# Kernel tuning notes

Measured on AMD Instinct MI355X. Metric: run time of the kernel, lower is better.

The kernel has to match this reference:

```python
import jax, jax.numpy as jnp
import numpy as np
from jax import lax

EPS = 1e-4  # BatchNorm eps from the module

def maxpool2x2(x):
    # x: [N, C, H, W] -> 2x2 max pool, stride 2, no padding
    return lax.reduce_window(x, -jnp.inf, lax.max, (1, 1, 2, 2), (1, 1, 2, 2), 'VALID')

def conv_nchw(x, w):
    return lax.conv_general_dilated(x, w, window_strides=(1, 1), padding='VALID',
                                    dimension_numbers=('NCHW', 'OIHW', 'NCHW'))

def setup_inputs() -> dict:
    key = jax.random.key(0)
    ks = jax.random.split(key, 6)
    return {
        'x':       jax.random.normal(ks[0], (8192, 1, 32, 32), dtype=jnp.float32),
        'conv1_w': jax.random.normal(ks[1], (20, 1, 5, 5), dtype=jnp.float32) * 0.1,
        'conv2_w': jax.random.normal(ks[2], (50, 20, 5, 5), dtype=jnp.float32) * 0.1,
        'lin_w':   jax.random.normal(ks[3], (500, 1250), dtype=jnp.float32) * 0.05,
        'fc_w':    jax.random.normal(ks[4], (10, 500), dtype=jnp.float32) * 0.05,
        'fc_b':    jax.random.normal(ks[5], (10,), dtype=jnp.float32) * 0.05,
    }

def reference(x, conv1_w, conv2_w, lin_w, fc_w, fc_b):
    # --- features ---
    # Conv2d(1, 20, k=5, bias=False): [N,1,32,32] -> [N,20,28,28]
    h = conv_nchw(x, conv1_w)
    # BatchNorm2d(20, eps=1e-4, affine=False), training-mode batch stats (biased var)
    mean = jnp.mean(h, axis=(0, 2, 3), keepdims=True)
    var = jnp.var(h, axis=(0, 2, 3), keepdims=True)
    h = (h - mean) * lax.rsqrt(var + EPS)
    # ReLU + MaxPool 2x2: -> [N,20,14,14]
    h = maxpool2x2(jnp.maximum(h, 0.0))
    # Binarize(): sign of activations
    h = jnp.sign(h)
    # Conv2dBinary(20, 50, k=5): XNOR-style conv = conv with sign(W), scaled by
    # per-output-channel alpha = mean(|W|). -> [N,50,10,10]
    alpha2 = jnp.mean(jnp.abs(conv2_w), axis=(1, 2, 3)).reshape(1, -1, 1, 1)
    h = conv_nchw(h, jnp.sign(conv2_w)) * alpha2
    # Hardtanh + MaxPool 2x2: -> [N,50,5,5]
    h = maxpool2x2(jnp.clip(h, -1.0, 1.0))
    # --- dense ---
    h = h.reshape(h.shape[0], -1)  # [N, 1250], channel-major like torch.flatten
    h = jnp.sign(h)
    # LinearBinary(1250, 500): y = x @ sign(W)^T * alpha, alpha = mean(|W|, dim=1)
    alpha_l = jnp.mean(jnp.abs(lin_w), axis=1)  # [500]
    h = (h @ jnp.sign(lin_w).T) * alpha_l
    h = jnp.clip(h, -1.0, 1.0)
    # fc: Linear(500, num_classes)
    return h @ fc_w.T + fc_b
```

## Files before the change

kernel.cpp:

```cpp
#include <hip/hip_runtime.h>
#include <stdint.h>


#define NIMG 8192

typedef __attribute__((ext_vector_type(8))) _Float16 f16x8;
typedef __attribute__((ext_vector_type(16))) float f32x16;
typedef __attribute__((ext_vector_type(4))) int i32x4;
typedef __attribute__((ext_vector_type(16))) int i32x16;


__global__ __launch_bounds__(256) void prepsum_k(const float* __restrict__ lw,
                                                 const float* __restrict__ w2,
                                                 const float* __restrict__ x,
                                                 unsigned long long* __restrict__ lwp,
                                                 float* __restrict__ alpha,
                                                 i32x4* __restrict__ bg,
                                                 float* __restrict__ partial) {
  int b = blockIdx.x, tid = threadIdx.x;
  if (b < 125) {
    int wave = tid >> 6, lane = tid & 63;
    int j = b * 4 + wave;
    float pa = 0.f;
    for (int k = lane; k < 1250; k += 64) pa += fabsf(lw[j * 1250 + k]);
    for (int o = 32; o > 0; o >>= 1) pa += __shfl_down(pa, o, 64);
    if (lane == 0) alpha[j] = pa / 1250.0f;
    if (lane < 20) {
      unsigned long long m = 0;
      int base = j * 1250 + lane * 64;
      int lim = 1250 - lane * 64; if (lim > 64) lim = 64;
      for (int bb = 0; bb < lim; ++bb)
        if (lw[base + bb] > 0.f) m |= (1ull << bb);
      lwp[j * 20 + lane] = m;
    }
  } else if (b < 138) {
    int idx = (b - 125) * 256 + tid;
    if (idx < 3200) {
      int t = idx >> 7;
      int rem = idx & 127;
      int l = rem & 63;
      int nt = rem >> 6;
      int oc = nt * 32 + (l & 31);
      int hi = l >> 5;
      i32x4 o4;
#pragma unroll
      for (int wi = 0; wi < 4; ++wi) {
        int word = 0;
#pragma unroll
        for (int bb = 0; bb < 4; ++bb) {
          int k = hi * 16 + wi * 4 + bb;
          int v = 0;
          if (k < 20 && oc < 50)
            v = (w2[(oc * 20 + k) * 25 + t] > 0.f) ? 1 : -1;
          word |= (v & 0xff) << (8 * bb);
        }
        o4[wi] = word;
      }
      bg[idx] = o4;
    }
  } else {
    int sb = b - 138;
    const float4* xv = (const float4*)x + (size_t)sb * 16 * 256;
    float ax = 0.f, ay = 0.f, az = 0.f, aw = 0.f;
    for (int nn = 0; nn < 16; ++nn) {
      float4 v = xv[nn * 256 + tid];
      ax += v.x; ay += v.y; az += v.z; aw += v.w;
    }
    float4 r; r.x = ax; r.y = ay; r.z = az; r.w = aw;
    ((float4*)(partial + (size_t)sb * 1024))[tid] = r;
  }
}

__global__ __launch_bounds__(256) void reduce_k(const float* __restrict__ partial,
                                                float* __restrict__ partial2) {
  int b = blockIdx.x, tid = threadIdx.x;
  int e = (b & 3) * 256 + tid;
  int p0 = (b >> 2) * 32;
  float s = 0.f;
#pragma unroll
  for (int p = 0; p < 32; ++p) s += partial[(size_t)(p0 + p) * 1024 + e];
  partial2[(size_t)(b >> 2) * 1024 + e] = s;
}

__global__ __launch_bounds__(256) void mean_k(const float* __restrict__ partial2,
                                              const float* __restrict__ w1,
                                              float* __restrict__ mean) {
  __shared__ float Tsh[1024];
  __shared__ double U8[25][8];
  __shared__ double U[25];
  int t = threadIdx.x;
  for (int e = t; e < 1024; e += 256) {
    double s = 0.0;
#pragma unroll
    for (int b = 0; b < 16; ++b) s += (double)partial2[b * 1024 + e];
    Tsh[e] = (float)s;
  }
  __syncthreads();
  if (t < 200) {
    int tap = t >> 3, part = t & 7;
    int ky = tap / 5, kx = tap % 5;
    double s = 0.0;
    for (int p = part * 98; p < part * 98 + 98; ++p) {
      int py = p / 28, px = p % 28;
      s += (double)Tsh[(py + ky) * 32 + px + kx];
    }
    U8[tap][part] = s;
  }
  __syncthreads();
  if (t < 25) {
    double s = 0.0;
    for (int i = 0; i < 8; ++i) s += U8[t][i];
    U[t] = s;
  }
  __syncthreads();
  if (t < 20) {
    double s = 0.0;
    for (int q = 0; q < 25; ++q) s += (double)w1[t * 25 + q] * U[q];
    mean[t] = (float)(s / (8192.0 * 784.0));
  }
}

__device__ inline uint32_t pack_f16_pair(float fv) {
  _Float16 h = (_Float16)fv;
  float rem = fv - (float)h;
  _Float16 l = (_Float16)(rem * 4096.0f);
  uint32_t hb = (uint32_t)__builtin_bit_cast(unsigned short, h);
  uint32_t lb = (uint32_t)__builtin_bit_cast(unsigned short, l);
  return (hb << 16) | lb;
}

__global__ __launch_bounds__(512, 4) void conv12_k(const float* __restrict__ x,
                                                   const float* __restrict__ w1,
                                                   const float* __restrict__ mean,
                                                   const i32x4* __restrict__ bg,
                                                   const unsigned long long* __restrict__ lwp,
                                                   const float* __restrict__ alpha,
                                                   const float* __restrict__ fcw,
                                                   const float* __restrict__ fcb,
                                                   float* __restrict__ out) {
  __shared__ uint32_t xs8[8][1032];
  __shared__ uint32_t b1sh[1568];
  __shared__ __attribute__((aligned(16))) char uni[8][2048];
  int tid = threadIdx.x;
  int wave = tid >> 6, lane = tid & 63;
  int n0 = blockIdx.x * 8;
  int n = n0 + wave;

  uint32_t* xs = xs8[wave];
  {
    const float4* xin = (const float4*)(x + (size_t)n * 1024);
#pragma unroll
    for (int i = 0; i < 4; ++i) {
      int idx = i * 64 + lane;
      float4 v = xin[idx];
      float fv[4] = {v.x, v.y, v.z, v.w};
#pragma unroll
      for (int e = 0; e < 4; ++e)
        xs[4 * idx + e] = pack_f16_pair(fv[e]);
    }
    if (lane < 8) xs[1024 + lane] = 0;
  }

  int bc = lane & 31;
  int khsel = lane >> 5;
  {
    f16x8 Bh[2], Bhs[2], Bl[2];
    const int t1tab[8] = {8, 9, 18, 19, 20, 21, 22, 23};
    const _Float16 SC = (_Float16)4096.0f;
#pragma unroll
    for (int j = 0; j < 8; ++j) {
      int t0 = j + khsel * 10;
      float wv0 = (bc < 20) ? w1[bc * 25 + t0] : 0.f;
      uint32_t p0 = pack_f16_pair(wv0);
      _Float16 h0 = __builtin_bit_cast(_Float16, (unsigned short)(p0 >> 16));
      Bh[0][j] = h0;
      Bhs[0][j] = h0 * SC;
      Bl[0][j] = __builtin_bit_cast(_Float16, (unsigned short)(p0 & 0xffffu));
      float wv1 = 0.f;
      if (bc < 20) {
        if (khsel == 0) wv1 = w1[bc * 25 + t1tab[j]];
        else if (j == 4) wv1 = w1[bc * 25 + 24];
      }
      uint32_t p1 = pack_f16_pair(wv1);
      _Float16 h1 = __builtin_bit_cast(_Float16, (unsigned short)(p1 >> 16));
      Bh[1][j] = h1;
      Bhs[1][j] = h1 * SC;
      Bl[1][j] = __builtin_bit_cast(_Float16, (unsigned short)(p1 & 0xffffu));
    }
    float mv = (bc < 20) ? mean[bc] * 4096.0f : 3.0e38f;

    int m = lane & 31;
    int d0 = m + khsel * 64;
    int d1 = m + khsel * 4;

    for (int pp = 0; pp < 14; ++pp) {
      unsigned long long bacc[16];
#pragma unroll
      for (int r = 0; r < 16; ++r) bacc[r] = 0ull;
#pragma unroll
      for (int py2 = 0; py2 < 2; ++py2) {
        int pybase = (2 * pp + py2) * 32;
        const uint32_t* b0 = xs + pybase + d0;
        const uint32_t* b1 = xs + pybase + d1;
        uint32_t raw[16];
        raw[0] = b0[0];   raw[1] = b0[1];   raw[2] = b0[2];   raw[3] = b0[3];
        raw[4] = b0[4];   raw[5] = b0[32];  raw[6] = b0[33];  raw[7] = b0[34];
        raw[8] = b1[35];  raw[9] = b1[36];  raw[10] = b1[99]; raw[11] = b1[100];
        raw[12] = b1[128]; raw[13] = b1[129]; raw[14] = b1[130]; raw[15] = b1[131];
        f16x8 Ah[2], Al[2];
#pragma unroll
        for (int kh = 0; kh < 2; ++kh) {
          uint32_t hw[4], lw2[4];
#pragma unroll
          for (int jj = 0; jj < 4; ++jj) {
            uint32_t v0 = raw[kh * 8 + 2 * jj], v1 = raw[kh * 8 + 2 * jj + 1];
            hw[jj] = __builtin_amdgcn_perm(v1, v0, 0x07060302u);
            lw2[jj] = __builtin_amdgcn_perm(v1, v0, 0x05040100u);
          }
          struct U4 { uint32_t a, b, c, d; };
          U4 hv4 = {hw[0], hw[1], hw[2], hw[3]};
          U4 lv4 = {lw2[0], lw2[1], lw2[2], lw2[3]};
          Ah[kh] = __builtin_bit_cast(f16x8, hv4);
          Al[kh] = __builtin_bit_cast(f16x8, lv4);
        }
        f32x16 acc;
#pragma unroll
        for (int i = 0; i < 16; ++i) acc[i] = 0.f;
        acc = __builtin_amdgcn_mfma_f32_32x32x16_f16(Ah[0], Bhs[0], acc, 0, 0, 0);
        acc = __builtin_amdgcn_mfma_f32_32x32x16_f16(Ah[1], Bhs[1], acc, 0, 0, 0);
        acc = __builtin_amdgcn_mfma_f32_32x32x16_f16(Ah[0], Bl[0], acc, 0, 0, 0);
        acc = __builtin_amdgcn_mfma_f32_32x32x16_f16(Ah[1], Bl[1], acc, 0, 0, 0);
        acc = __builtin_amdgcn_mfma_f32_32x32x16_f16(Al[0], Bh[0], acc, 0, 0, 0);
        acc = __builtin_amdgcn_mfma_f32_32x32x16_f16(Al[1], Bh[1], acc, 0, 0, 0);
#pragma unroll
        for (int r = 0; r < 16; ++r)
          bacc[r] |= __ballot(acc[r] > mv);
      }
      uint32_t pm = 0;
#pragma unroll
      for (int pc = 0; pc < 14; ++pc) {
        int px0 = 2 * pc;
        int r0 = (px0 & 3) + 4 * (px0 >> 3);
        int h0 = (px0 >> 2) & 1;
        unsigned long long mm = bacc[r0] | bacc[r0 + 1];
        uint32_t val = (uint32_t)(mm >> (32 * h0));
        if (lane == pc) pm = val;
      }
      if (lane < 14) b1sh[wave * 196 + pp * 14 + lane] = pm;
    }
  }
  __syncthreads();

  {
    int m = lane & 31, hi = lane >> 5;
    int shbase = hi * 16;
    for (int mt = wave; mt < 25; mt += 8) {
      int qg = mt * 8 + (m >> 2);
      int img = (qg * 41) >> 10;
      int quad = qg - img * 25;
      int Y = (quad * 13) >> 6;
      int X = quad - Y * 5;
      int px = (2 * Y + ((m >> 1) & 1)) * 14 + 2 * X + (m & 1);
      const uint32_t* arow = b1sh + img * 196 + px;
      const i32x4* bgl = bg + lane;
      i32x16 acc0, acc1;
#pragma unroll
      for (int i = 0; i < 16; ++i) { acc0[i] = 0; acc1[i] = 0; }
#pragma unroll 1
      for (int ky = 0; ky < 5; ++ky) {
        const uint32_t* ar2 = arow + ky * 14;
        const i32x4* bg2 = bgl + ky * 5 * 128;
#pragma unroll
        for (int kx = 0; kx < 5; ++kx) {
          uint32_t w = ar2[kx];
          i32x4 av;
#pragma unroll
          for (int wi = 0; wi < 4; ++wi)
            av[wi] = (int)((((w >> (shbase + 4 * wi)) & 0xFu) * 0x00204081u) & 0x01010101u);
          i32x4 bv0 = bg2[kx * 128];
          i32x4 bv1 = bg2[kx * 128 + 64];
          acc0 = __builtin_amdgcn_mfma_i32_32x32x32_i8(av, bv0, acc0, 0, 0, 0);
          acc1 = __builtin_amdgcn_mfma_i32_32x32x32_i8(av, bv1, acc1, 0, 0, 0);
        }
      }
      int oc0 = m, oc1 = 32 + m;
#pragma unroll
      for (int g = 0; g < 4; ++g) {
        int qloc = 2 * g + hi;
        int qg2 = mt * 8 + qloc;
        int img2 = (qg2 * 41) >> 10;
        int quad2 = qg2 - img2 * 25;
        {
          int a0 = acc0[4 * g], a1 = acc0[4 * g + 1], a2 = acc0[4 * g + 2], a3 = acc0[4 * g + 3];
          int c0 = a0 > a1 ? a0 : a1, c1 = a2 > a3 ? a2 : a3;
          int best = c0 > c1 ? c0 : c1;
          uni[img2][oc0 * 25 + quad2] = (char)((best > 0) - (best < 0));
        }
        if (oc1 < 50) {
          int a0 = acc1[4 * g], a1 = acc1[4 * g + 1], a2 = acc1[4 * g + 2], a3 = acc1[4 * g + 3];
          int c0 = a0 > a1 ? a0 : a1, c1 = a2 > a3 ? a2 : a3;
          int best = c0 > c1 ? c0 : c1;
          uni[img2][oc1 * 25 + quad2] = (char)((best > 0) - (best < 0));
        }
      }
    }
  }
  __syncthreads();

  signed char* s2w = (signed char*)uni[wave];
  float* hshw = (float*)uni[wave];
  if (lane < 30) s2w[1250 + lane] = 0;

  unsigned long long Pm[20], Nm[20];
  int cp = 0, cn = 0;
#pragma unroll
  for (int k = 0; k < 20; ++k) {
    signed char v = s2w[k * 64 + lane];
    unsigned long long P = __ballot(v > 0);
    unsigned long long N = __ballot(v < 0);
    Pm[k] = P; Nm[k] = N;
    cp += __popcll(P); cn += __popcll(N);
  }

#pragma unroll
  for (int rd = 0; rd < 8; ++rd) {
    int j = rd * 64 + lane;
    float y = 0.f;
    if (j < 500) {
      const ulonglong2* W2 = (const ulonglong2*)(lwp + (size_t)j * 20);
      int a = 0, b = 0;
#pragma unroll
      for (int i = 0; i < 10; ++i) {
        ulonglong2 w2v = W2[i];
        a += __popcll(w2v.x & Pm[2 * i]) + __popcll(w2v.y & Pm[2 * i + 1]);
        b += __popcll(w2v.x & Nm[2 * i]) + __popcll(w2v.y & Nm[2 * i + 1]);
      }
      int dot = 2 * (a - b) - cp + cn;
      y = alpha[j] * (float)dot;
      y = fminf(1.0f, fmaxf(-1.0f, y));
    }
    hshw[rd * 64 + lane] = y;
  }

  float hv[8];
#pragma unroll
  for (int k = 0; k < 8; ++k) hv[k] = hshw[k * 64 + lane];
#pragma unroll
  for (int o = 0; o < 10; ++o) {
    float pa = 0.f;
#pragma unroll
    for (int k = 0; k < 8; ++k) {
      int j = k * 64 + lane;
      if (j < 500) pa += hv[k] * fcw[o * 500 + j];
    }
    for (int off = 32; off > 0; off >>= 1) pa += __shfl_down(pa, off, 64);
    if (lane == 0) out[(size_t)n * 10 + o] = pa + fcb[o];
  }
}

extern "C" void kernel_launch(void* const* d_in, const int* in_sizes, int n_in,
                              void* d_out, int out_size, void* d_ws, size_t ws_size,
                              hipStream_t stream) {
  const float* x   = (const float*)d_in[0];
  const float* w1  = (const float*)d_in[1];
  const float* w2  = (const float*)d_in[2];
  const float* lw  = (const float*)d_in[3];
  const float* fcw = (const float*)d_in[4];
  const float* fcb = (const float*)d_in[5];
  float* out = (float*)d_out;
  char* ws = (char*)d_ws;

  float*    mean  = (float*)(ws + 0);
  float*    alpha = (float*)(ws + 5632);
  unsigned long long* lwp = (unsigned long long*)(ws + 7680);
  float*    partial = (float*)(ws + 87808);
  float*    partial2 = (float*)(ws + 8607488);
  i32x4*    bg    = (i32x4*)(ws + 8673024);

  prepsum_k<<<650, 256, 0, stream>>>(lw, w2, x, lwp, alpha, bg, partial);
  reduce_k<<<64, 256, 0, stream>>>(partial, partial2);
  mean_k<<<1, 256, 0, stream>>>(partial2, w1, mean);
  conv12_k<<<1024, 512, 0, stream>>>(x, w1, mean, bg, lwp, alpha, fcw, fcb, out);
}
```

Measured before the change: 219.4 us.

## Drop reduce kernel, widen partial sums, ballot-pack weights, split MFMA chains

Each pre-pass block now sums 64 images instead of 16, which cuts the partial sums to 128 rows. The single mean kernel reduces those rows directly, so the intermediate reduce launch is removed. The sign bits of the linear weights are now built with wave ballots inside the coalesced |W| loop, replacing a serial per-lane bit loop. In conv12 the six dependent MFMAs are split across two accumulators to shorten the dependency chain, at the cost of an extra add per element before the ballot and a longer serial reduction in mean_k.

```diff
diff --git a/kernel.cpp b/kernel.cpp
--- a/kernel.cpp
+++ b/kernel.cpp
@@ -22,17 +22,16 @@
     int wave = tid >> 6, lane = tid & 63;
     int j = b * 4 + wave;
     float pa = 0.f;
-    for (int k = lane; k < 1250; k += 64) pa += fabsf(lw[j * 1250 + k]);
+#pragma unroll
+    for (int w = 0; w < 20; ++w) {
+      int idx = w * 64 + lane;
+      float v = (idx < 1250) ? lw[j * 1250 + idx] : 0.f;
+      pa += fabsf(v);
+      unsigned long long m = __ballot(v > 0.f);
+      if (lane == 0) lwp[j * 20 + w] = m;
+    }
     for (int o = 32; o > 0; o >>= 1) pa += __shfl_down(pa, o, 64);
     if (lane == 0) alpha[j] = pa / 1250.0f;
-    if (lane < 20) {
-      unsigned long long m = 0;
-      int base = j * 1250 + lane * 64;
-      int lim = 1250 - lane * 64; if (lim > 64) lim = 64;
-      for (int bb = 0; bb < lim; ++bb)
-        if (lw[base + bb] > 0.f) m |= (1ull << bb);
-      lwp[j * 20 + lane] = m;
-    }
   } else if (b < 138) {
     int idx = (b - 125) * 256 + tid;
     if (idx < 3200) {
@@ -60,9 +59,9 @@
     }
   } else {
     int sb = b - 138;
-    const float4* xv = (const float4*)x + (size_t)sb * 16 * 256;
+    const float4* xv = (const float4*)x + (size_t)sb * 64 * 256;
     float ax = 0.f, ay = 0.f, az = 0.f, aw = 0.f;
-    for (int nn = 0; nn < 16; ++nn) {
+    for (int nn = 0; nn < 64; ++nn) {
       float4 v = xv[nn * 256 + tid];
       ax += v.x; ay += v.y; az += v.z; aw += v.w;
     }
@@ -71,18 +70,7 @@
   }
 }
 
-__global__ __launch_bounds__(256) void reduce_k(const float* __restrict__ partial,
-                                                float* __restrict__ partial2) {
-  int b = blockIdx.x, tid = threadIdx.x;
-  int e = (b & 3) * 256 + tid;
-  int p0 = (b >> 2) * 32;
-  float s = 0.f;
-#pragma unroll
-  for (int p = 0; p < 32; ++p) s += partial[(size_t)(p0 + p) * 1024 + e];
-  partial2[(size_t)(b >> 2) * 1024 + e] = s;
-}
-
-__global__ __launch_bounds__(256) void mean_k(const float* __restrict__ partial2,
+__global__ __launch_bounds__(256) void mean_k(const float* __restrict__ partial,
                                               const float* __restrict__ w1,
                                               float* __restrict__ mean) {
   __shared__ float Tsh[1024];
@@ -91,8 +79,7 @@
   int t = threadIdx.x;
   for (int e = t; e < 1024; e += 256) {
     double s = 0.0;
-#pragma unroll
-    for (int b = 0; b < 16; ++b) s += (double)partial2[b * 1024 + e];
+    for (int b = 0; b < 128; ++b) s += (double)partial[(size_t)b * 1024 + e];
     Tsh[e] = (float)s;
   }
   __syncthreads();
@@ -223,18 +210,18 @@
           Ah[kh] = __builtin_bit_cast(f16x8, hv4);
           Al[kh] = __builtin_bit_cast(f16x8, lv4);
         }
-        f32x16 acc;
-#pragma unroll
-        for (int i = 0; i < 16; ++i) acc[i] = 0.f;
-        acc = __builtin_amdgcn_mfma_f32_32x32x16_f16(Ah[0], Bhs[0], acc, 0, 0, 0);
-        acc = __builtin_amdgcn_mfma_f32_32x32x16_f16(Ah[1], Bhs[1], acc, 0, 0, 0);
-        acc = __builtin_amdgcn_mfma_f32_32x32x16_f16(Ah[0], Bl[0], acc, 0, 0, 0);
-        acc = __builtin_amdgcn_mfma_f32_32x32x16_f16(Ah[1], Bl[1], acc, 0, 0, 0);
-        acc = __builtin_amdgcn_mfma_f32_32x32x16_f16(Al[0], Bh[0], acc, 0, 0, 0);
-        acc = __builtin_amdgcn_mfma_f32_32x32x16_f16(Al[1], Bh[1], acc, 0, 0, 0);
+        f32x16 acc, acc2;
+#pragma unroll
+        for (int i = 0; i < 16; ++i) { acc[i] = 0.f; acc2[i] = 0.f; }
+        acc  = __builtin_amdgcn_mfma_f32_32x32x16_f16(Ah[0], Bhs[0], acc, 0, 0, 0);
+        acc2 = __builtin_amdgcn_mfma_f32_32x32x16_f16(Ah[1], Bhs[1], acc2, 0, 0, 0);
+        acc  = __builtin_amdgcn_mfma_f32_32x32x16_f16(Ah[0], Bl[0], acc, 0, 0, 0);
+        acc2 = __builtin_amdgcn_mfma_f32_32x32x16_f16(Ah[1], Bl[1], acc2, 0, 0, 0);
+        acc  = __builtin_amdgcn_mfma_f32_32x32x16_f16(Al[0], Bh[0], acc, 0, 0, 0);
+        acc2 = __builtin_amdgcn_mfma_f32_32x32x16_f16(Al[1], Bh[1], acc2, 0, 0, 0);
 #pragma unroll
         for (int r = 0; r < 16; ++r)
-          bacc[r] |= __ballot(acc[r] > mv);
+          bacc[r] |= __ballot(acc[r] + acc2[r] > mv);
       }
       uint32_t pm = 0;
 #pragma unroll
@@ -374,11 +361,9 @@
   float*    alpha = (float*)(ws + 5632);
   unsigned long long* lwp = (unsigned long long*)(ws + 7680);
   float*    partial = (float*)(ws + 87808);
-  float*    partial2 = (float*)(ws + 8607488);
   i32x4*    bg    = (i32x4*)(ws + 8673024);
 
-  prepsum_k<<<650, 256, 0, stream>>>(lw, w2, x, lwp, alpha, bg, partial);
-  reduce_k<<<64, 256, 0, stream>>>(partial, partial2);
-  mean_k<<<1, 256, 0, stream>>>(partial2, w1, mean);
+  prepsum_k<<<266, 256, 0, stream>>>(lw, w2, x, lwp, alpha, bg, partial);
+  mean_k<<<1, 256, 0, stream>>>(partial, w1, mean);
   conv12_k<<<1024, 512, 0, stream>>>(x, w1, mean, bg, lwp, alpha, fcw, fcb, out);
 }
```

Result: slower. 224.5 us (+2.3%).
